# Kernel optimization log

Hardware: AMD Instinct MI355X
Metric: run time of the kernel (lower is better)

## Reference

```python
import jax, jax.numpy as jnp
import numpy as np

IN_F, HID, OUT_F, N_HEADS, BATCH = 256, 512, 2048, 8, 4096


def _kaiming_uniform(key, shape, fan_in):
    # kaiming_uniform_ with a=sqrt(5): gain = sqrt(2/(1+5)) = 1/sqrt(3)
    gain = 1.0 / np.sqrt(3.0)
    bound = gain * np.sqrt(3.0 / fan_in)  # = sqrt(1/fan_in)
    return jax.random.uniform(key, shape, jnp.float32, -bound, bound)


def setup_inputs() -> dict:
    key = jax.random.key(0)
    kx, ki, k1, k2, k3, k4 = jax.random.split(key, 6)
    X = jax.random.normal(kx, (BATCH, IN_F), jnp.float32)
    X_head_idx = jax.random.randint(ki, (BATCH,), 0, N_HEADS)
    # layer 1: in -> hidden
    W1 = _kaiming_uniform(k1, (N_HEADS, IN_F, HID), IN_F)
    b1 = jax.random.uniform(k2, (N_HEADS, HID), jnp.float32,
                            -1.0 / np.sqrt(IN_F), 1.0 / np.sqrt(IN_F))
    # layer 2: hidden -> out
    W2 = _kaiming_uniform(k3, (N_HEADS, HID, OUT_F), HID)
    b2 = jax.random.uniform(k4, (N_HEADS, OUT_F), jnp.float32,
                            -1.0 / np.sqrt(HID), 1.0 / np.sqrt(HID))
    return {"X": X, "X_head_idx": X_head_idx, "W1": W1, "b1": b1,
            "W2": W2, "b2": b2}


def _selective_linear(x, idx, W, b):
    # x: [B, in], W: [H, in, out], b: [H, out], idx: [B]
    # compute all heads densely, then select each sample's head
    y = jnp.einsum('bi,hio->bho', x, W) + b[None]   # [B, H, out]
    return jnp.take_along_axis(y, idx[:, None, None], axis=1)[:, 0, :]


def reference(X, X_head_idx, W1, b1, W2, b2):
    h = _selective_linear(X, X_head_idx, W1, b1)
    h = jax.nn.relu(h)
    out = _selective_linear(h, X_head_idx, W2, b2)
    return out
```

## Files before the change

### kernel.cpp

```cpp
#include <hip/hip_runtime.h>

#define IN_F 256
#define HID 512
#define OUT_F 2048
#define N_HEADS 8
#define BATCH 4096
#define MT 40

typedef __bf16 bf16_t;
typedef bf16_t bf16x8 __attribute__((ext_vector_type(8)));
typedef float f32x4 __attribute__((ext_vector_type(4)));

typedef __attribute__((address_space(1))) const unsigned int gu32;
typedef __attribute__((address_space(3))) unsigned int lu32;

__device__ inline unsigned short f2bf(float f) {
  union { float f; unsigned u; } v; v.f = f;
  unsigned u = v.u;
  unsigned r = (u + 0x7FFFu + ((u >> 16) & 1u)) >> 16;
  return (unsigned short)r;
}

__device__ __forceinline__ bool map_tile(const int* offsets, int my,
                                         int& head, int& row0, int& rows) {
  head = -1;
  int acc_t = 0;
#pragma unroll
  for (int h = 0; h < N_HEADS; ++h) {
    int o0 = offsets[h], o1 = offsets[h + 1];
    int cnt = o1 - o0;
    int t = (cnt + 127) >> 7;
    if (head < 0 && my < acc_t + t) {
      head = h;
      int lt = my - acc_t;
      row0 = o0 + lt * 128;
      rows = min(128, cnt - lt * 128);
    }
    acc_t += t;
  }
  return head >= 0;
}

__device__ __forceinline__ void bucket_body(const int* __restrict__ idxh,
                                            int* __restrict__ order,
                                            int* __restrict__ offsets,
                                            char* smem, int tid) {
  int* cnt = (int*)smem;
  int* basep = cnt + 8;
  int* cur = basep + 9;
  if (tid < N_HEADS) cnt[tid] = 0;
  __syncthreads();
  for (int i = tid; i < BATCH; i += 256) atomicAdd(&cnt[idxh[i]], 1);
  __syncthreads();
  if (tid == 0) {
    int a = 0;
#pragma unroll
    for (int h = 0; h < N_HEADS; ++h) { basep[h] = a; cur[h] = a; a += cnt[h]; }
    basep[N_HEADS] = a;
  }
  __syncthreads();
  if (tid < N_HEADS + 1) offsets[tid] = basep[tid];
  for (int i = tid; i < BATCH; i += 256) {
    int pos = atomicAdd(&cur[idxh[i]], 1);
    order[pos] = i;
  }
}

__device__ __forceinline__ void transpose_one(const float* __restrict__ W,
                                              unsigned short* __restrict__ Wt,
                                              int K, int N, int b, int nt,
                                              char* smem, int tid) {
  float (*tile)[65] = (float(*)[65])smem;
  int c = tid & 63, r0 = tid >> 6;
  int per_head = nt * (K / 64);
  int h = b / per_head, rem = b % per_head;
  int n0 = (rem % nt) * 64, k0 = (rem / nt) * 64;
  const float* Wh = W + (size_t)h * K * N;
  unsigned short* Wth = Wt + (size_t)h * K * N;
  for (int rr = r0; rr < 64; rr += 4)
    tile[rr][c] = Wh[(size_t)(k0 + rr) * N + n0 + c];
  __syncthreads();
  for (int rr = r0; rr < 64; rr += 4)
    Wth[(size_t)(n0 + rr) * K + k0 + c] = f2bf(tile[c][rr]);
}

__device__ __forceinline__ void gemm1_tile(const float* __restrict__ X,
                                           const int* __restrict__ order,
                                           const unsigned short* __restrict__ W1t,
                                           const float* __restrict__ b1,
                                           unsigned short* __restrict__ Hb,
                                           int head, int row0, int rows, int n0,
                                           char* smem, int tid) {
  unsigned short* As = (unsigned short*)smem;
  unsigned short* Bs = (unsigned short*)(smem + 8192);
  int wave = tid >> 6, lane = tid & 63;
  int q = lane >> 4, l16 = lane & 15;
  int w_m = wave >> 1, w_n = wave & 1;
  int ldrow = lane >> 2, ldcol = (lane & 3) * 8;
  int c0 = wave * 2, c1 = c0 + 1;
  int arow = tid >> 1, acolh = (tid & 1) * 16;

  const unsigned short* Bh = W1t + (size_t)head * HID * IN_F;
  const unsigned short* bp0 = Bh + (size_t)(n0 + c0 * 16 + ldrow) * IN_F + ldcol;
  const unsigned short* bp1 = Bh + (size_t)(n0 + c1 * 16 + ldrow) * IN_F + ldcol;
  unsigned short* lB0 = Bs + c0 * 512;
  unsigned short* lB1 = Bs + c1 * 512;
  int src = order[row0 + min(arow, rows - 1)];
  const float* xrow = X + (size_t)src * IN_F + acolh;
  unsigned short* aw = As + arow * 32 + acolh;

  f32x4 acc[4][4];
#pragma unroll
  for (int i = 0; i < 4; ++i)
#pragma unroll
    for (int j = 0; j < 4; ++j) acc[i][j] = (f32x4){0.f, 0.f, 0.f, 0.f};

  for (int k0 = 0; k0 < IN_F; k0 += 32) {
    __builtin_amdgcn_global_load_lds((gu32*)bp0, (lu32*)lB0, 16, 0, 0);
    __builtin_amdgcn_global_load_lds((gu32*)bp1, (lu32*)lB1, 16, 0, 0);
    bp0 += 32; bp1 += 32;
    const float4* xp = (const float4*)(xrow + k0);
    float4 f0 = xp[0], f1 = xp[1], f2 = xp[2], f3 = xp[3];
    uint4 o0, o1;
    o0.x = (unsigned)f2bf(f0.x) | ((unsigned)f2bf(f0.y) << 16);
    o0.y = (unsigned)f2bf(f0.z) | ((unsigned)f2bf(f0.w) << 16);
    o0.z = (unsigned)f2bf(f1.x) | ((unsigned)f2bf(f1.y) << 16);
    o0.w = (unsigned)f2bf(f1.z) | ((unsigned)f2bf(f1.w) << 16);
    o1.x = (unsigned)f2bf(f2.x) | ((unsigned)f2bf(f2.y) << 16);
    o1.y = (unsigned)f2bf(f2.z) | ((unsigned)f2bf(f2.w) << 16);
    o1.z = (unsigned)f2bf(f3.x) | ((unsigned)f2bf(f3.y) << 16);
    o1.w = (unsigned)f2bf(f3.z) | ((unsigned)f2bf(f3.w) << 16);
    *(uint4*)aw = o0;
    *(uint4*)(aw + 8) = o1;
    __syncthreads();

    bf16x8 af[4], bfr[4];
#pragma unroll
    for (int i = 0; i < 4; ++i) {
      af[i] = *(const bf16x8*)(As + (w_m * 64 + i * 16 + l16) * 32 + q * 8);
      bfr[i] = *(const bf16x8*)(Bs + (w_n * 64 + i * 16 + l16) * 32 + q * 8);
    }
#pragma unroll
    for (int mi = 0; mi < 4; ++mi)
#pragma unroll
      for (int ni = 0; ni < 4; ++ni)
        acc[mi][ni] = __builtin_amdgcn_mfma_f32_16x16x32_bf16(af[mi], bfr[ni], acc[mi][ni], 0, 0, 0);
    __syncthreads();
  }

  float bval[4];
#pragma unroll
  for (int ni = 0; ni < 4; ++ni)
    bval[ni] = b1[(size_t)head * HID + n0 + w_n * 64 + ni * 16 + l16];
#pragma unroll
  for (int mi = 0; mi < 4; ++mi) {
#pragma unroll
    for (int r = 0; r < 4; ++r) {
      int m = w_m * 64 + mi * 16 + q * 4 + r;
      if (m < rows) {
        int p = row0 + m;
#pragma unroll
        for (int ni = 0; ni < 4; ++ni) {
          int n = n0 + w_n * 64 + ni * 16 + l16;
          float v = acc[mi][ni][r] + bval[ni];
          v = v > 0.f ? v : 0.f;
          Hb[(size_t)p * HID + n] = f2bf(v);
        }
      }
    }
  }
}

__device__ __forceinline__ void gemm2_tile(const unsigned short* __restrict__ Hb,
                                           const unsigned short* __restrict__ W2t,
                                           const float* __restrict__ b2,
                                           const int* __restrict__ order,
                                           float* __restrict__ out,
                                           int head, int row0, int rows, int n0,
                                           char* smem, int tid) {
  unsigned short* As = (unsigned short*)smem;
  unsigned short* Bs = (unsigned short*)(smem + 8192);
  int wave = tid >> 6, lane = tid & 63;
  int q = lane >> 4, l16 = lane & 15;
  int w_m = wave >> 1, w_n = wave & 1;
  int ldrow = lane >> 2, ldcol = (lane & 3) * 8;
  int c0 = wave * 2, c1 = c0 + 1;

  const unsigned short* Bh = W2t + (size_t)head * (size_t)OUT_F * HID;
  int ar0 = row0 + min(c0 * 16 + ldrow, rows - 1);
  int ar1 = row0 + min(c1 * 16 + ldrow, rows - 1);
  const unsigned short* ap0 = Hb + (size_t)ar0 * HID + ldcol;
  const unsigned short* ap1 = Hb + (size_t)ar1 * HID + ldcol;
  const unsigned short* bp0 = Bh + (size_t)(n0 + c0 * 16 + ldrow) * HID + ldcol;
  const unsigned short* bp1 = Bh + (size_t)(n0 + c1 * 16 + ldrow) * HID + ldcol;
  unsigned short* lA0 = As + c0 * 512;
  unsigned short* lA1 = As + c1 * 512;
  unsigned short* lB0 = Bs + c0 * 512;
  unsigned short* lB1 = Bs + c1 * 512;

  f32x4 acc[4][4];
#pragma unroll
  for (int i = 0; i < 4; ++i)
#pragma unroll
    for (int j = 0; j < 4; ++j) acc[i][j] = (f32x4){0.f, 0.f, 0.f, 0.f};

  for (int k0 = 0; k0 < HID; k0 += 32) {
    __builtin_amdgcn_global_load_lds((gu32*)ap0, (lu32*)lA0, 16, 0, 0);
    __builtin_amdgcn_global_load_lds((gu32*)ap1, (lu32*)lA1, 16, 0, 0);
    __builtin_amdgcn_global_load_lds((gu32*)bp0, (lu32*)lB0, 16, 0, 0);
    __builtin_amdgcn_global_load_lds((gu32*)bp1, (lu32*)lB1, 16, 0, 0);
    ap0 += 32; ap1 += 32; bp0 += 32; bp1 += 32;
    __syncthreads();

    bf16x8 af[4], bfr[4];
#pragma unroll
    for (int i = 0; i < 4; ++i) {
      af[i] = *(const bf16x8*)(As + (w_m * 64 + i * 16 + l16) * 32 + q * 8);
      bfr[i] = *(const bf16x8*)(Bs + (w_n * 64 + i * 16 + l16) * 32 + q * 8);
    }
#pragma unroll
    for (int mi = 0; mi < 4; ++mi)
#pragma unroll
      for (int ni = 0; ni < 4; ++ni)
        acc[mi][ni] = __builtin_amdgcn_mfma_f32_16x16x32_bf16(af[mi], bfr[ni], acc[mi][ni], 0, 0, 0);
    __syncthreads();
  }

  float bval[4];
#pragma unroll
  for (int ni = 0; ni < 4; ++ni)
    bval[ni] = b2[(size_t)head * OUT_F + n0 + w_n * 64 + ni * 16 + l16];
#pragma unroll
  for (int mi = 0; mi < 4; ++mi) {
#pragma unroll
    for (int r = 0; r < 4; ++r) {
      int m = w_m * 64 + mi * 16 + q * 4 + r;
      if (m < rows) {
        int rg = order[row0 + m];
#pragma unroll
        for (int ni = 0; ni < 4; ++ni) {
          int n = n0 + w_n * 64 + ni * 16 + l16;
          out[(size_t)rg * OUT_F + n] = acc[mi][ni][r] + bval[ni];
        }
      }
    }
  }
}

__global__ __launch_bounds__(256) void prep1_kernel(const int* __restrict__ idxh,
                                                    int* order, int* offsets,
                                                    const float* __restrict__ W1,
                                                    unsigned short* __restrict__ W1t) {
  __shared__ __align__(16) char smem[16640];
  int tid = threadIdx.x;
  int b = blockIdx.x;
  if (b == 0) {
    bucket_body(idxh, order, offsets, smem, tid);
  } else {
    transpose_one(W1, W1t, IN_F, HID, b - 1, HID / 64, smem, tid);
  }
}

__global__ __launch_bounds__(256) void mid_kernel(const float* __restrict__ X,
                                                  const int* __restrict__ order,
                                                  const int* __restrict__ offsets,
                                                  const unsigned short* __restrict__ W1t,
                                                  const float* __restrict__ b1,
                                                  unsigned short* __restrict__ Hb,
                                                  const float* __restrict__ W2,
                                                  unsigned short* __restrict__ W2t) {
  __shared__ __align__(16) char smem[16640];
  int tid = threadIdx.x;
  int b = blockIdx.x;
  if (b < MT * 4) {
    int my = b >> 2, nx = b & 3;
    int head, row0, rows;
    if (!map_tile(offsets, my, head, row0, rows)) return;
    gemm1_tile(X, order, W1t, b1, Hb, head, row0, rows, nx * 128, smem, tid);
  } else {
    transpose_one(W2, W2t, HID, OUT_F, b - MT * 4, OUT_F / 64, smem, tid);
  }
}

__global__ __launch_bounds__(256) void gemm2_kernel(const unsigned short* __restrict__ Hb,
                                                    const unsigned short* __restrict__ W2t,
                                                    const float* __restrict__ b2,
                                                    const int* __restrict__ offsets,
                                                    const int* __restrict__ order,
                                                    float* __restrict__ out) {
  __shared__ __align__(16) char smem[16384];
  int head, row0, rows;
  if (!map_tile(offsets, blockIdx.y, head, row0, rows)) return;
  gemm2_tile(Hb, W2t, b2, order, out, head, row0, rows, blockIdx.x * 128, smem, threadIdx.x);
}

extern "C" void kernel_launch(void* const* d_in, const int* in_sizes, int n_in,
                              void* d_out, int out_size, void* d_ws, size_t ws_size,
                              hipStream_t stream) {
  const float* X = (const float*)d_in[0];
  const int* idxh = (const int*)d_in[1];
  const float* W1 = (const float*)d_in[2];
  const float* b1 = (const float*)d_in[3];
  const float* W2 = (const float*)d_in[4];
  const float* b2 = (const float*)d_in[5];
  float* out = (float*)d_out;

  char* ws = (char*)d_ws;
  int* order = (int*)ws;                     ws += (size_t)BATCH * 4;
  int* offsets = (int*)ws;                   ws += 64;
  unsigned short* W1t = (unsigned short*)ws; ws += (size_t)N_HEADS * IN_F * HID * 2;
  unsigned short* W2t = (unsigned short*)ws; ws += (size_t)N_HEADS * HID * OUT_F * 2;
  unsigned short* Hb = (unsigned short*)ws;  ws += (size_t)BATCH * HID * 2;

  prep1_kernel<<<dim3(1 + 256), dim3(256), 0, stream>>>(idxh, order, offsets, W1, W1t);
  mid_kernel<<<dim3(MT * 4 + 2048), dim3(256), 0, stream>>>(X, order, offsets, W1t, b1, Hb, W2, W2t);
  gemm2_kernel<<<dim3(OUT_F / 128, MT), dim3(256), 0, stream>>>(Hb, W2t, b2, offsets, order, out);
}
```

Baseline: 138.0 us.

## Parallelize bucketing, merge weight transposes, double-buffer GEMM tiles via registers

Replaces the single-block serial bucketing with 16 blocks using global atomics into per-head order arrays, with counts cleared by a memset. Both weight transposes move into one prep kernel, so gemm1 becomes its own launch instead of sharing a kernel with the W2 transpose. Both GEMMs swap direct global-to-LDS loads for register prefetch into double-buffered LDS, which drops one barrier per k-step. The cost is an extra memset launch and more registers and LDS per block; row order within a head becomes nondeterministic, which does not affect the output.

```diff
diff --git a/kernel.cpp b/kernel.cpp
--- a/kernel.cpp
+++ b/kernel.cpp
@@ -11,103 +11,108 @@
 typedef bf16_t bf16x8 __attribute__((ext_vector_type(8)));
 typedef float f32x4 __attribute__((ext_vector_type(4)));
 
-typedef __attribute__((address_space(1))) const unsigned int gu32;
-typedef __attribute__((address_space(3))) unsigned int lu32;
-
-__device__ inline unsigned short f2bf(float f) {
+__device__ inline unsigned f2bf(float f) {
   union { float f; unsigned u; } v; v.f = f;
   unsigned u = v.u;
-  unsigned r = (u + 0x7FFFu + ((u >> 16) & 1u)) >> 16;
-  return (unsigned short)r;
-}
-
-__device__ __forceinline__ bool map_tile(const int* offsets, int my,
-                                         int& head, int& row0, int& rows) {
+  return (u + 0x7FFFu + ((u >> 16) & 1u)) >> 16;
+}
+
+__device__ inline uint4 pack8(float4 f0, float4 f1) {
+  uint4 o;
+  o.x = f2bf(f0.x) | (f2bf(f0.y) << 16);
+  o.y = f2bf(f0.z) | (f2bf(f0.w) << 16);
+  o.z = f2bf(f1.x) | (f2bf(f1.y) << 16);
+  o.w = f2bf(f1.z) | (f2bf(f1.w) << 16);
+  return o;
+}
+
+__device__ __forceinline__ bool map_tile(const int* cnt, int my, int& head,
+                                         int& hbase, int& row0, int& rows) {
   head = -1;
-  int acc_t = 0;
+  int acc_t = 0, bsum = 0;
 #pragma unroll
   for (int h = 0; h < N_HEADS; ++h) {
-    int o0 = offsets[h], o1 = offsets[h + 1];
-    int cnt = o1 - o0;
-    int t = (cnt + 127) >> 7;
+    int c = cnt[h];
+    int t = (c + 127) >> 7;
     if (head < 0 && my < acc_t + t) {
       head = h;
       int lt = my - acc_t;
-      row0 = o0 + lt * 128;
-      rows = min(128, cnt - lt * 128);
+      row0 = lt * 128;
+      rows = min(128, c - row0);
+      hbase = bsum;
     }
     acc_t += t;
+    bsum += c;
   }
   return head >= 0;
 }
 
-__device__ __forceinline__ void bucket_body(const int* __restrict__ idxh,
-                                            int* __restrict__ order,
-                                            int* __restrict__ offsets,
-                                            char* smem, int tid) {
-  int* cnt = (int*)smem;
-  int* basep = cnt + 8;
-  int* cur = basep + 9;
-  if (tid < N_HEADS) cnt[tid] = 0;
-  __syncthreads();
-  for (int i = tid; i < BATCH; i += 256) atomicAdd(&cnt[idxh[i]], 1);
-  __syncthreads();
-  if (tid == 0) {
-    int a = 0;
-#pragma unroll
-    for (int h = 0; h < N_HEADS; ++h) { basep[h] = a; cur[h] = a; a += cnt[h]; }
-    basep[N_HEADS] = a;
-  }
-  __syncthreads();
-  if (tid < N_HEADS + 1) offsets[tid] = basep[tid];
-  for (int i = tid; i < BATCH; i += 256) {
-    int pos = atomicAdd(&cur[idxh[i]], 1);
-    order[pos] = i;
-  }
-}
-
-__device__ __forceinline__ void transpose_one(const float* __restrict__ W,
-                                              unsigned short* __restrict__ Wt,
-                                              int K, int N, int b, int nt,
-                                              char* smem, int tid) {
-  float (*tile)[65] = (float(*)[65])smem;
-  int c = tid & 63, r0 = tid >> 6;
+__global__ __launch_bounds__(256) void prep_kernel(const int* __restrict__ idxh,
+                                                   int* __restrict__ order_h,
+                                                   int* __restrict__ cnt,
+                                                   const float* __restrict__ W1,
+                                                   unsigned short* __restrict__ W1t,
+                                                   const float* __restrict__ W2,
+                                                   unsigned short* __restrict__ W2t) {
+  __shared__ float tile[64][65];
+  int tid = threadIdx.x;
+  int b = blockIdx.x;
+  if (b < 16) {
+    int i = b * 256 + tid;
+    int h = idxh[i];
+    int pos = atomicAdd(&cnt[h], 1);
+    order_h[h * BATCH + pos] = i;
+    return;
+  }
+  const float* W; unsigned short* Wt; int K, N, t;
+  if (b < 272) { W = W1; Wt = W1t; K = IN_F; N = HID; t = b - 16; }
+  else { W = W2; Wt = W2t; K = HID; N = OUT_F; t = b - 272; }
+  int nt = N / 64;
   int per_head = nt * (K / 64);
-  int h = b / per_head, rem = b % per_head;
+  int h = t / per_head, rem = t % per_head;
   int n0 = (rem % nt) * 64, k0 = (rem / nt) * 64;
   const float* Wh = W + (size_t)h * K * N;
   unsigned short* Wth = Wt + (size_t)h * K * N;
+  int c = tid & 63, r0 = tid >> 6;
   for (int rr = r0; rr < 64; rr += 4)
     tile[rr][c] = Wh[(size_t)(k0 + rr) * N + n0 + c];
   __syncthreads();
   for (int rr = r0; rr < 64; rr += 4)
-    Wth[(size_t)(n0 + rr) * K + k0 + c] = f2bf(tile[c][rr]);
-}
-
-__device__ __forceinline__ void gemm1_tile(const float* __restrict__ X,
-                                           const int* __restrict__ order,
-                                           const unsigned short* __restrict__ W1t,
-                                           const float* __restrict__ b1,
-                                           unsigned short* __restrict__ Hb,
-                                           int head, int row0, int rows, int n0,
-                                           char* smem, int tid) {
-  unsigned short* As = (unsigned short*)smem;
-  unsigned short* Bs = (unsigned short*)(smem + 8192);
+    Wth[(size_t)(n0 + rr) * K + k0 + c] = (unsigned short)f2bf(tile[c][rr]);
+}
+
+__global__ __launch_bounds__(256) void gemm1_kernel(const float* __restrict__ X,
+                                                    const int* __restrict__ order_h,
+                                                    const int* __restrict__ cnt,
+                                                    const unsigned short* __restrict__ W1t,
+                                                    const float* __restrict__ b1,
+                                                    unsigned short* __restrict__ Hb) {
+  __shared__ __align__(16) unsigned short As[2][128 * 32];
+  __shared__ __align__(16) unsigned short Bs[2][128 * 32];
+  int head, hbase, row0, rows;
+  if (!map_tile(cnt, blockIdx.y, head, hbase, row0, rows)) return;
+  int n0 = blockIdx.x * 128;
+  int tid = threadIdx.x;
   int wave = tid >> 6, lane = tid & 63;
   int q = lane >> 4, l16 = lane & 15;
   int w_m = wave >> 1, w_n = wave & 1;
   int ldrow = lane >> 2, ldcol = (lane & 3) * 8;
   int c0 = wave * 2, c1 = c0 + 1;
-  int arow = tid >> 1, acolh = (tid & 1) * 16;
-
+  int lofs0 = c0 * 512 + lane * 8;
+  int lofs1 = c1 * 512 + lane * 8;
+
+  int xr0 = order_h[head * BATCH + row0 + min(c0 * 16 + ldrow, rows - 1)];
+  int xr1 = order_h[head * BATCH + row0 + min(c1 * 16 + ldrow, rows - 1)];
+  const float* xp0 = X + (size_t)xr0 * IN_F + ldcol;
+  const float* xp1 = X + (size_t)xr1 * IN_F + ldcol;
   const unsigned short* Bh = W1t + (size_t)head * HID * IN_F;
   const unsigned short* bp0 = Bh + (size_t)(n0 + c0 * 16 + ldrow) * IN_F + ldcol;
   const unsigned short* bp1 = Bh + (size_t)(n0 + c1 * 16 + ldrow) * IN_F + ldcol;
-  unsigned short* lB0 = Bs + c0 * 512;
-  unsigned short* lB1 = Bs + c1 * 512;
-  int src = order[row0 + min(arow, rows - 1)];
-  const float* xrow = X + (size_t)src * IN_F + acolh;
-  unsigned short* aw = As + arow * 32 + acolh;
+
+  float4 fa0 = *(const float4*)xp0, fa1 = *(const float4*)(xp0 + 4);
+  float4 fb0 = *(const float4*)xp1, fb1 = *(const float4*)(xp1 + 4);
+  uint4 bv0 = *(const uint4*)bp0, bv1 = *(const uint4*)bp1;
+  xp0 += 32; xp1 += 32; bp0 += 32; bp1 += 32;
 
   f32x4 acc[4][4];
 #pragma unroll
@@ -115,37 +120,35 @@
 #pragma unroll
     for (int j = 0; j < 4; ++j) acc[i][j] = (f32x4){0.f, 0.f, 0.f, 0.f};
 
-  for (int k0 = 0; k0 < IN_F; k0 += 32) {
-    __builtin_amdgcn_global_load_lds((gu32*)bp0, (lu32*)lB0, 16, 0, 0);
-    __builtin_amdgcn_global_load_lds((gu32*)bp1, (lu32*)lB1, 16, 0, 0);
-    bp0 += 32; bp1 += 32;
-    const float4* xp = (const float4*)(xrow + k0);
-    float4 f0 = xp[0], f1 = xp[1], f2 = xp[2], f3 = xp[3];
-    uint4 o0, o1;
-    o0.x = (unsigned)f2bf(f0.x) | ((unsigned)f2bf(f0.y) << 16);
-    o0.y = (unsigned)f2bf(f0.z) | ((unsigned)f2bf(f0.w) << 16);
-    o0.z = (unsigned)f2bf(f1.x) | ((unsigned)f2bf(f1.y) << 16);
-    o0.w = (unsigned)f2bf(f1.z) | ((unsigned)f2bf(f1.w) << 16);
-    o1.x = (unsigned)f2bf(f2.x) | ((unsigned)f2bf(f2.y) << 16);
-    o1.y = (unsigned)f2bf(f2.z) | ((unsigned)f2bf(f2.w) << 16);
-    o1.z = (unsigned)f2bf(f3.x) | ((unsigned)f2bf(f3.y) << 16);
-    o1.w = (unsigned)f2bf(f3.z) | ((unsigned)f2bf(f3.w) << 16);
-    *(uint4*)aw = o0;
-    *(uint4*)(aw + 8) = o1;
+  constexpr int KIT = IN_F / 32;
+  for (int k = 0; k < KIT; ++k) {
+    int cur = k & 1;
+    *(uint4*)(As[cur] + lofs0) = pack8(fa0, fa1);
+    *(uint4*)(As[cur] + lofs1) = pack8(fb0, fb1);
+    *(uint4*)(Bs[cur] + lofs0) = bv0;
+    *(uint4*)(Bs[cur] + lofs1) = bv1;
+    float4 nfa0, nfa1, nfb0, nfb1; uint4 nbv0, nbv1;
+    if (k < KIT - 1) {
+      nfa0 = *(const float4*)xp0; nfa1 = *(const float4*)(xp0 + 4);
+      nfb0 = *(const float4*)xp1; nfb1 = *(const float4*)(xp1 + 4);
+      nbv0 = *(const uint4*)bp0;  nbv1 = *(const uint4*)bp1;
+      xp0 += 32; xp1 += 32; bp0 += 32; bp1 += 32;
+    }
     __syncthreads();
-
     bf16x8 af[4], bfr[4];
 #pragma unroll
     for (int i = 0; i < 4; ++i) {
-      af[i] = *(const bf16x8*)(As + (w_m * 64 + i * 16 + l16) * 32 + q * 8);
-      bfr[i] = *(const bf16x8*)(Bs + (w_n * 64 + i * 16 + l16) * 32 + q * 8);
+      af[i] = *(const bf16x8*)(As[cur] + (w_m * 64 + i * 16 + l16) * 32 + q * 8);
+      bfr[i] = *(const bf16x8*)(Bs[cur] + (w_n * 64 + i * 16 + l16) * 32 + q * 8);
     }
 #pragma unroll
     for (int mi = 0; mi < 4; ++mi)
 #pragma unroll
       for (int ni = 0; ni < 4; ++ni)
         acc[mi][ni] = __builtin_amdgcn_mfma_f32_16x16x32_bf16(af[mi], bfr[ni], acc[mi][ni], 0, 0, 0);
-    __syncthreads();
+    if (k < KIT - 1) {
+      fa0 = nfa0; fa1 = nfa1; fb0 = nfb0; fb1 = nfb1; bv0 = nbv0; bv1 = nbv1;
+    }
   }
 
   float bval[4];
@@ -158,45 +161,50 @@
     for (int r = 0; r < 4; ++r) {
       int m = w_m * 64 + mi * 16 + q * 4 + r;
       if (m < rows) {
-        int p = row0 + m;
+        int p = hbase + row0 + m;
 #pragma unroll
         for (int ni = 0; ni < 4; ++ni) {
           int n = n0 + w_n * 64 + ni * 16 + l16;
           float v = acc[mi][ni][r] + bval[ni];
           v = v > 0.f ? v : 0.f;
-          Hb[(size_t)p * HID + n] = f2bf(v);
+          Hb[(size_t)p * HID + n] = (unsigned short)f2bf(v);
         }
       }
     }
   }
 }
 
-__device__ __forceinline__ void gemm2_tile(const unsigned short* __restrict__ Hb,
-                                           const unsigned short* __restrict__ W2t,
-                                           const float* __restrict__ b2,
-                                           const int* __restrict__ order,
-                                           float* __restrict__ out,
-                                           int head, int row0, int rows, int n0,
-                                           char* smem, int tid) {
-  unsigned short* As = (unsigned short*)smem;
-  unsigned short* Bs = (unsigned short*)(smem + 8192);
+__global__ __launch_bounds__(256) void gemm2_kernel(const unsigned short* __restrict__ Hb,
+                                                    const unsigned short* __restrict__ W2t,
+                                                    const float* __restrict__ b2,
+                                                    const int* __restrict__ cnt,
+                                                    const int* __restrict__ order_h,
+                                                    float* __restrict__ out) {
+  __shared__ __align__(16) unsigned short As[2][128 * 32];
+  __shared__ __align__(16) unsigned short Bs[2][128 * 32];
+  int head, hbase, row0, rows;
+  if (!map_tile(cnt, blockIdx.y, head, hbase, row0, rows)) return;
+  int n0 = blockIdx.x * 128;
+  int tid = threadIdx.x;
   int wave = tid >> 6, lane = tid & 63;
   int q = lane >> 4, l16 = lane & 15;
   int w_m = wave >> 1, w_n = wave & 1;
   int ldrow = lane >> 2, ldcol = (lane & 3) * 8;
   int c0 = wave * 2, c1 = c0 + 1;
-
-  const unsigned short* Bh = W2t + (size_t)head * (size_t)OUT_F * HID;
-  int ar0 = row0 + min(c0 * 16 + ldrow, rows - 1);
-  int ar1 = row0 + min(c1 * 16 + ldrow, rows - 1);
+  int lofs0 = c0 * 512 + lane * 8;
+  int lofs1 = c1 * 512 + lane * 8;
+
+  int ar0 = hbase + row0 + min(c0 * 16 + ldrow, rows - 1);
+  int ar1 = hbase + row0 + min(c1 * 16 + ldrow, rows - 1);
   const unsigned short* ap0 = Hb + (size_t)ar0 * HID + ldcol;
   const unsigned short* ap1 = Hb + (size_t)ar1 * HID + ldcol;
+  const unsigned short* Bh = W2t + (size_t)head * (size_t)OUT_F * HID;
   const unsigned short* bp0 = Bh + (size_t)(n0 + c0 * 16 + ldrow) * HID + ldcol;
   const unsigned short* bp1 = Bh + (size_t)(n0 + c1 * 16 + ldrow) * HID + ldcol;
-  unsigned short* lA0 = As + c0 * 512;
-  unsigned short* lA1 = As + c1 * 512;
-  unsigned short* lB0 = Bs + c0 * 512;
-  unsigned short* lB1 = Bs + c1 * 512;
+
+  uint4 av0 = *(const uint4*)ap0, av1 = *(const uint4*)ap1;
+  uint4 bv0 = *(const uint4*)bp0, bv1 = *(const uint4*)bp1;
+  ap0 += 32; ap1 += 32; bp0 += 32; bp1 += 32;
 
   f32x4 acc[4][4];
 #pragma unroll
@@ -204,26 +212,32 @@
 #pragma unroll
     for (int j = 0; j < 4; ++j) acc[i][j] = (f32x4){0.f, 0.f, 0.f, 0.f};
 
-  for (int k0 = 0; k0 < HID; k0 += 32) {
-    __builtin_amdgcn_global_load_lds((gu32*)ap0, (lu32*)lA0, 16, 0, 0);
-    __builtin_amdgcn_global_load_lds((gu32*)ap1, (lu32*)lA1, 16, 0, 0);
-    __builtin_amdgcn_global_load_lds((gu32*)bp0, (lu32*)lB0, 16, 0, 0);
-    __builtin_amdgcn_global_load_lds((gu32*)bp1, (lu32*)lB1, 16, 0, 0);
-    ap0 += 32; ap1 += 32; bp0 += 32; bp1 += 32;
+  constexpr int KIT = HID / 32;
+  for (int k = 0; k < KIT; ++k) {
+    int cur = k & 1;
+    *(uint4*)(As[cur] + lofs0) = av0;
+    *(uint4*)(As[cur] + lofs1) = av1;
+    *(uint4*)(Bs[cur] + lofs0) = bv0;
+    *(uint4*)(Bs[cur] + lofs1) = bv1;
+    uint4 nav0, nav1, nbv0, nbv1;
+    if (k < KIT - 1) {
+      nav0 = *(const uint4*)ap0; nav1 = *(const uint4*)ap1;
+      nbv0 = *(const uint4*)bp0; nbv1 = *(const uint4*)bp1;
+      ap0 += 32; ap1 += 32; bp0 += 32; bp1 += 32;
+    }
     __syncthreads();
-
     bf16x8 af[4], bfr[4];
 #pragma unroll
     for (int i = 0; i < 4; ++i) {
-      af[i] = *(const bf16x8*)(As + (w_m * 64 + i * 16 + l16) * 32 + q * 8);
-      bfr[i] = *(const bf16x8*)(Bs + (w_n * 64 + i * 16 + l16) * 32 + q * 8);
+      af[i] = *(const bf16x8*)(As[cur] + (w_m * 64 + i * 16 + l16) * 32 + q * 8);
+      bfr[i] = *(const bf16x8*)(Bs[cur] + (w_n * 64 + i * 16 + l16) * 32 + q * 8);
     }
 #pragma unroll
     for (int mi = 0; mi < 4; ++mi)
 #pragma unroll
       for (int ni = 0; ni < 4; ++ni)
         acc[mi][ni] = __builtin_amdgcn_mfma_f32_16x16x32_bf16(af[mi], bfr[ni], acc[mi][ni], 0, 0, 0);
-    __syncthreads();
+    if (k < KIT - 1) { av0 = nav0; av1 = nav1; bv0 = nbv0; bv1 = nbv1; }
   }
 
   float bval[4];
@@ -236,7 +250,7 @@
     for (int r = 0; r < 4; ++r) {
       int m = w_m * 64 + mi * 16 + q * 4 + r;
       if (m < rows) {
-        int rg = order[row0 + m];
+        int rg = order_h[head * BATCH + row0 + m];
 #pragma unroll
         for (int ni = 0; ni < 4; ++ni) {
           int n = n0 + w_n * 64 + ni * 16 + l16;
@@ -245,53 +259,6 @@
       }
     }
   }
-}
-
-__global__ __launch_bounds__(256) void prep1_kernel(const int* __restrict__ idxh,
-                                                    int* order, int* offsets,
-                                                    const float* __restrict__ W1,
-                                                    unsigned short* __restrict__ W1t) {
-  __shared__ __align__(16) char smem[16640];
-  int tid = threadIdx.x;
-  int b = blockIdx.x;
-  if (b == 0) {
-    bucket_body(idxh, order, offsets, smem, tid);
-  } else {
-    transpose_one(W1, W1t, IN_F, HID, b - 1, HID / 64, smem, tid);
-  }
-}
-
-__global__ __launch_bounds__(256) void mid_kernel(const float* __restrict__ X,
-                                                  const int* __restrict__ order,
-                                                  const int* __restrict__ offsets,
-                                                  const unsigned short* __restrict__ W1t,
-                                                  const float* __restrict__ b1,
-                                                  unsigned short* __restrict__ Hb,
-                                                  const float* __restrict__ W2,
-                                                  unsigned short* __restrict__ W2t) {
-  __shared__ __align__(16) char smem[16640];
-  int tid = threadIdx.x;
-  int b = blockIdx.x;
-  if (b < MT * 4) {
-    int my = b >> 2, nx = b & 3;
-    int head, row0, rows;
-    if (!map_tile(offsets, my, head, row0, rows)) return;
-    gemm1_tile(X, order, W1t, b1, Hb, head, row0, rows, nx * 128, smem, tid);
-  } else {
-    transpose_one(W2, W2t, HID, OUT_F, b - MT * 4, OUT_F / 64, smem, tid);
-  }
-}
-
-__global__ __launch_bounds__(256) void gemm2_kernel(const unsigned short* __restrict__ Hb,
-                                                    const unsigned short* __restrict__ W2t,
-                                                    const float* __restrict__ b2,
-                                                    const int* __restrict__ offsets,
-                                                    const int* __restrict__ order,
-                                                    float* __restrict__ out) {
-  __shared__ __align__(16) char smem[16384];
-  int head, row0, rows;
-  if (!map_tile(offsets, blockIdx.y, head, row0, rows)) return;
-  gemm2_tile(Hb, W2t, b2, order, out, head, row0, rows, blockIdx.x * 128, smem, threadIdx.x);
 }
 
 extern "C" void kernel_launch(void* const* d_in, const int* in_sizes, int n_in,
@@ -306,13 +273,15 @@
   float* out = (float*)d_out;
 
   char* ws = (char*)d_ws;
-  int* order = (int*)ws;                     ws += (size_t)BATCH * 4;
-  int* offsets = (int*)ws;                   ws += 64;
+  int* order_h = (int*)ws;                   ws += (size_t)N_HEADS * BATCH * 4;
+  int* cnt = (int*)ws;                       ws += 64;
   unsigned short* W1t = (unsigned short*)ws; ws += (size_t)N_HEADS * IN_F * HID * 2;
   unsigned short* W2t = (unsigned short*)ws; ws += (size_t)N_HEADS * HID * OUT_F * 2;
   unsigned short* Hb = (unsigned short*)ws;  ws += (size_t)BATCH * HID * 2;
 
-  prep1_kernel<<<dim3(1 + 256), dim3(256), 0, stream>>>(idxh, order, offsets, W1, W1t);
-  mid_kernel<<<dim3(MT * 4 + 2048), dim3(256), 0, stream>>>(X, order, offsets, W1t, b1, Hb, W2, W2t);
-  gemm2_kernel<<<dim3(OUT_F / 128, MT), dim3(256), 0, stream>>>(Hb, W2t, b2, offsets, order, out);
-}
+  (void)hipMemsetAsync(cnt, 0, 64, stream);
+  prep_kernel<<<dim3(16 + 256 + 2048), dim3(256), 0, stream>>>(idxh, order_h, cnt,
+                                                               W1, W1t, W2, W2t);
+  gemm1_kernel<<<dim3(HID / 128, MT), dim3(256), 0, stream>>>(X, order_h, cnt, W1t, b1, Hb);
+  gemm2_kernel<<<dim3(OUT_F / 128, MT), dim3(256), 0, stream>>>(Hb, W2t, b2, cnt, order_h, out);
+}
```

After: 141.9 us. 2.8% more time.
